# Optimization experiments

Measured on AMD Instinct MI355X. Metric: run time of the kernel, lower is better.

The kernel has to match this reference:

```python
import jax, jax.numpy as jnp
import numpy as np

B = 131072
D_IN = 385          # 384-d embedding + 1 correctness feature
D_H = 192           # both trunk layers resolve to max(.,192)=192 per source
Q = 1000            # number of questions
C = 16              # classes per head (uniform padding of per-question heads)


def setup_inputs() -> dict:
    key = jax.random.key(0)
    ks = jax.random.split(key, 9)
    x = jax.random.normal(ks[0], (B, D_IN), dtype=jnp.float32)
    question_ids = jax.random.randint(ks[1], (B,), 0, Q, dtype=jnp.int32)
    is_correct = jax.random.randint(ks[2], (B,), 0, 2, dtype=jnp.int32)
    W1 = jax.random.normal(ks[3], (D_IN, D_H), dtype=jnp.float32) * 0.05
    b1 = jnp.zeros((D_H,), dtype=jnp.float32)
    W2 = jax.random.normal(ks[4], (D_H, D_H), dtype=jnp.float32) * 0.05
    b2 = jnp.zeros((D_H,), dtype=jnp.float32)
    # Head bank: slots [0,Q) = false heads, [Q,2Q) = true heads.
    W_heads = jax.random.normal(ks[5], (2 * Q, C, D_H), dtype=jnp.float32) * 0.05
    b_heads = jax.random.normal(ks[6], (2 * Q, C), dtype=jnp.float32) * 0.05
    return {"x": x, "question_ids": question_ids, "is_correct": is_correct,
            "W1": W1, "b1": b1, "W2": W2, "b2": b2,
            "W_heads": W_heads, "b_heads": b_heads}


def reference(x, question_ids, is_correct, W1, b1, W2, b2, W_heads, b_heads):
    # Shared trunk (eval mode: dropout = identity)
    h = jax.nn.relu(x @ W1 + b1)            # [B, 192]
    feat = jax.nn.relu(h @ W2 + b2)         # [B, 192]
    # Hard routing: pick true or false head for this question.
    Qn = W_heads.shape[0] // 2
    idx = question_ids + is_correct * Qn    # [B]
    Wq = W_heads[idx]                       # [B, C, 192] gather (memory-bound)
    bq = b_heads[idx]                       # [B, C]
    logits = jnp.einsum('bcd,bd->bc', Wq, feat) + bq  # per-sample routed linear
    return logits
```

## Files before the change

### kernel.cpp

```cpp
#include <hip/hip_runtime.h>
#include <hip/hip_bf16.h>
#include <stdint.h>
#include <stddef.h>


typedef short s8v __attribute__((ext_vector_type(8)));
typedef float f4v __attribute__((ext_vector_type(4)));
typedef float f4a __attribute__((ext_vector_type(4), aligned(4)));

typedef const void __attribute__((address_space(1))) *gas1_t;
typedef void __attribute__((address_space(3))) *las3_t;

namespace {
constexpr int kDin = 385;
constexpr int kDh  = 192;
constexpr int kQ   = 1000;
constexpr int kC   = 16;
constexpr int BM   = 64;
constexpr int NT   = 256;
constexpr int NK1  = 13;
constexpr int NK2  = 6;
constexpr int CHUNK = 12 * 64 * 8;
constexpr int H2   = 200;

constexpr size_t WS_W1   = 0;
constexpr size_t WS_W2   = 163840;
constexpr size_t WS_HIST = 245760;
constexpr size_t WS_CUR  = 253952;
constexpr size_t WS_PERM = 262144;
}

__device__ __forceinline__ unsigned short f2bf(float f) {
  unsigned int u = __float_as_uint(f);
  u = u + 0x7fffu + ((u >> 16) & 1u);
  return (unsigned short)(u >> 16);
}

__device__ __forceinline__ unsigned int pk2(float lo, float hi) {
  union { __hip_bfloat162 h2; unsigned int u; } cv;
  cv.h2 = __float22bfloat162_rn(make_float2(lo, hi));
  return cv.u;
}

union s8u { s8v s; unsigned int u[4]; };

__device__ __forceinline__ void swz_one(const float* W, int K, int i,
                                        unsigned short* out) {
  int k = i / kDh;
  int c = i - k * kDh;
  float v = (k < K) ? W[(size_t)k * kDh + c] : 0.f;
  int oi = (k >> 5) * CHUNK + (((c >> 4) * 64 + ((k >> 3) & 3) * 16 + (c & 15)) << 3)
         + (k & 7);
  out[oi] = f2bf(v);
}

__global__ void combo_prep(const int* __restrict__ qid, const int* __restrict__ isc,
                           int B, int nbH,
                           const float* __restrict__ W1, const float* __restrict__ W2,
                           int* __restrict__ hist,
                           unsigned short* __restrict__ W1sw,
                           unsigned short* __restrict__ W2sw) {
  int bid = blockIdx.x;
  if (bid < nbH) {
    int i = bid * 256 + threadIdx.x;
    if (i < B) atomicAdd(&hist[qid[i] + isc[i] * kQ], 1);
  } else if (bid < nbH + 312) {
    swz_one(W1, kDin, (bid - nbH) * 256 + threadIdx.x, W1sw);
  } else {
    swz_one(W2, kDh, (bid - nbH - 312) * 256 + threadIdx.x, W2sw);
  }
}

__global__ __launch_bounds__(256)
void scatter2(const int* __restrict__ qid, const int* __restrict__ isc, int B,
              const int* __restrict__ hist, int* __restrict__ rank_ctr,
              int* __restrict__ perm) {
  __shared__ int sh[2048];
  __shared__ int ssum[256];
  int t = threadIdx.x;
  int4 a = ((const int4*)hist)[t * 2];
  int4 b = ((const int4*)hist)[t * 2 + 1];
  int s1 = a.x + a.y, s2 = s1 + a.z, s3 = s2 + a.w;
  int s4 = s3 + b.x, s5 = s4 + b.y, s6 = s5 + b.z, s7 = s6 + b.w;
  ssum[t] = s7;
  __syncthreads();
  #pragma unroll
  for (int d = 1; d < 256; d <<= 1) {
    int xv = (t >= d) ? ssum[t - d] : 0;
    __syncthreads();
    ssum[t] += xv;
    __syncthreads();
  }
  int base = ssum[t] - s7;
  sh[t * 8 + 0] = base;
  sh[t * 8 + 1] = base + a.x;
  sh[t * 8 + 2] = base + s1;
  sh[t * 8 + 3] = base + s2;
  sh[t * 8 + 4] = base + s3;
  sh[t * 8 + 5] = base + s4;
  sh[t * 8 + 6] = base + s5;
  sh[t * 8 + 7] = base + s6;
  __syncthreads();
  int i = blockIdx.x * 256 + t;
  if (i < B) {
    int h = qid[i] + isc[i] * kQ;
    int pos = sh[h] + atomicAdd(&rank_ctr[h], 1);
    perm[pos] = i;
  }
}

__device__ __forceinline__ void stage_chunk(const unsigned short* gsrc,
                                            unsigned short* lbase, int tid) {
  const char* g = (const char*)gsrc + (size_t)tid * 16;
  char* l = (char*)lbase + ((tid >> 6) << 10);
  __builtin_amdgcn_global_load_lds((gas1_t)g,          (las3_t)l,          16, 0, 0);
  __builtin_amdgcn_global_load_lds((gas1_t)(g + 4096), (las3_t)(l + 4096), 16, 0, 0);
  __builtin_amdgcn_global_load_lds((gas1_t)(g + 8192), (las3_t)(l + 8192), 16, 0, 0);
}

__global__ __launch_bounds__(NT, 3)
void fused_qmlp6(const float* __restrict__ x,
                 const int*   __restrict__ qid,
                 const int*   __restrict__ isc,
                 const float* __restrict__ b1,
                 const float* __restrict__ b2,
                 const float* __restrict__ Wh,
                 const float* __restrict__ bh,
                 const unsigned short* __restrict__ W1sw,
                 const unsigned short* __restrict__ W2sw,
                 const int*   __restrict__ perm,
                 float* __restrict__ out) {
  __shared__ __align__(16) unsigned short hS[BM * H2];
  __shared__ __align__(16) unsigned short bS[2 * CHUNK];
  __shared__ int permS[BM];
  __shared__ int idxS[BM];

  const int tid  = threadIdx.x;
  const int lane = tid & 63, wid = tid >> 6;
  const int m = lane & 15, quad = lane >> 4;
  const int rh = wid & 1, ch = wid >> 1;
  const int row0 = blockIdx.x * BM;

  if (tid < BM) {
    int p = perm[row0 + tid];
    permS[tid] = p;
    idxS[tid] = qid[p] + isc[p] * kQ;
  }
  stage_chunk(W1sw, bS, tid);
  __syncthreads();

  const float* px0 = x + (size_t)permS[rh * 32 + m] * kDin;
  const float* px1 = x + (size_t)permS[rh * 32 + m + 16] * kDin;

  f4v acc0[6], acc1[6];
  #pragma unroll
  for (int t = 0; t < 6; ++t) {
    acc0[t] = (f4v){0.f, 0.f, 0.f, 0.f};
    acc1[t] = (f4v){0.f, 0.f, 0.f, 0.f};
  }

  f4a c0, c1, c2, c3;
  {
    const float* q0 = px0 + quad * 8;
    const float* q1 = px1 + quad * 8;
    c0 = *(const f4a*)q0; c1 = *(const f4a*)(q0 + 4);
    c2 = *(const f4a*)q1; c3 = *(const f4a*)(q1 + 4);
  }
  float tl0 = 0.f, tl1 = 0.f;

  #pragma unroll
  for (int kk = 0; kk < NK1; ++kk) {
    const int nj = kk + 1;
    const unsigned short* np = (nj < NK1)
        ? W1sw + (size_t)nj * CHUNK
        : W2sw;
    stage_chunk(np, bS + (nj & 1) * CHUNK, tid);

    f4a n0, n1, n2, n3;
    if (kk < NK1 - 2) {
      const float* q0 = px0 + nj * 32 + quad * 8;
      const float* q1 = px1 + nj * 32 + quad * 8;
      n0 = *(const f4a*)q0; n1 = *(const f4a*)(q0 + 4);
      n2 = *(const f4a*)q1; n3 = *(const f4a*)(q1 + 4);
    } else if (kk == NK1 - 2) {
      tl0 = (quad == 0) ? px0[384] : 0.f;
      tl1 = (quad == 0) ? px1[384] : 0.f;
    }

    s8v a0, a1;
    if (kk < NK1 - 1) {
      s8u ua, ub;
      ua.u[0] = pk2(c0[0], c0[1]); ua.u[1] = pk2(c0[2], c0[3]);
      ua.u[2] = pk2(c1[0], c1[1]); ua.u[3] = pk2(c1[2], c1[3]);
      ub.u[0] = pk2(c2[0], c2[1]); ub.u[1] = pk2(c2[2], c2[3]);
      ub.u[2] = pk2(c3[0], c3[1]); ub.u[3] = pk2(c3[2], c3[3]);
      a0 = ua.s; a1 = ub.s;
    } else {
      a0 = (s8v){0,0,0,0,0,0,0,0};
      a1 = (s8v){0,0,0,0,0,0,0,0};
      a0[0] = (short)f2bf(tl0);
      a1[0] = (short)f2bf(tl1);
    }

    const unsigned short* bBuf = bS + (kk & 1) * CHUNK;
    #pragma unroll
    for (int t = 0; t < 6; ++t) {
      s8v b = *(const s8v*)&bBuf[((ch * 6 + t) * 64 + lane) * 8];
      acc0[t] = __builtin_amdgcn_mfma_f32_16x16x32_bf16(a0, b, acc0[t], 0, 0, 0);
      acc1[t] = __builtin_amdgcn_mfma_f32_16x16x32_bf16(a1, b, acc1[t], 0, 0, 0);
    }
    __syncthreads();
    if (kk < NK1 - 2) { c0 = n0; c1 = n1; c2 = n2; c3 = n3; }
  }

  #pragma unroll
  for (int t = 0; t < 6; ++t) {
    int c = ch * 96 + t * 16 + m;
    float bb = b1[c];
    #pragma unroll
    for (int r4 = 0; r4 < 4; ++r4) {
      int r = rh * 32 + quad * 4 + r4;
      float v0 = acc0[t][r4] + bb; v0 = v0 > 0.f ? v0 : 0.f;
      hS[r * H2 + c] = f2bf(v0);
      float v1 = acc1[t][r4] + bb; v1 = v1 > 0.f ? v1 : 0.f;
      hS[(r + 16) * H2 + c] = f2bf(v1);
      acc0[t][r4] = 0.f;
      acc1[t][r4] = 0.f;
    }
  }
  __syncthreads();

  const int ar0 = (rh * 32 + m) * H2;
  #pragma unroll
  for (int k2 = 0; k2 < NK2; ++k2) {
    if (k2 < NK2 - 1)
      stage_chunk(W2sw + (size_t)(k2 + 1) * CHUNK,
                  bS + ((14 + k2) & 1) * CHUNK, tid);

    s8v a0 = *(const s8v*)&hS[ar0 + k2 * 32 + quad * 8];
    s8v a1 = *(const s8v*)&hS[ar0 + 16 * H2 + k2 * 32 + quad * 8];
    const unsigned short* bBuf = bS + ((13 + k2) & 1) * CHUNK;
    #pragma unroll
    for (int t = 0; t < 6; ++t) {
      s8v b = *(const s8v*)&bBuf[((ch * 6 + t) * 64 + lane) * 8];
      acc0[t] = __builtin_amdgcn_mfma_f32_16x16x32_bf16(a0, b, acc0[t], 0, 0, 0);
      acc1[t] = __builtin_amdgcn_mfma_f32_16x16x32_bf16(a1, b, acc1[t], 0, 0, 0);
    }
    __syncthreads();
  }

  #pragma unroll
  for (int t = 0; t < 6; ++t) {
    int c = ch * 96 + t * 16 + m;
    float bb = b2[c];
    #pragma unroll
    for (int r4 = 0; r4 < 4; ++r4) {
      int r = rh * 32 + quad * 4 + r4;
      float v0 = acc0[t][r4] + bb;
      hS[r * H2 + c] = f2bf(v0 > 0.f ? v0 : 0.f);
      float v1 = acc1[t][r4] + bb;
      hS[(r + 16) * H2 + c] = f2bf(v1 > 0.f ? v1 : 0.f);
    }
  }
  __syncthreads();

  {
    const int w16 = wid * 16;
    const int hm = idxS[w16 + m];
    unsigned rem = 0xFFFFu;
    while (rem) {
      int r0 = (int)__builtin_ctz(rem);
      int h = idxS[w16 + r0];
      unsigned long long bal = __ballot(hm == h);
      unsigned mask16 = (unsigned)(bal & 0xFFFFu);
      rem &= ~mask16;
      bool valid = (hm == h);

      const float* wq = Wh + ((size_t)h * kC + m) * kDh + quad * 8;
      f4v acc = (f4v){0.f, 0.f, 0.f, 0.f};
      #pragma unroll
      for (int kk = 0; kk < 6; ++kk) {
        float4 wlo = *(const float4*)(wq + kk * 32);
        float4 whi = *(const float4*)(wq + kk * 32 + 4);
        s8u ub;
        ub.u[0] = pk2(wlo.x, wlo.y);
        ub.u[1] = pk2(wlo.z, wlo.w);
        ub.u[2] = pk2(whi.x, whi.y);
        ub.u[3] = pk2(whi.z, whi.w);
        s8v bfr = ub.s;
        s8v afr = *(const s8v*)&hS[(w16 + m) * H2 + kk * 32 + quad * 8];
        if (!valid) afr = (s8v){0,0,0,0,0,0,0,0};
        acc = __builtin_amdgcn_mfma_f32_16x16x32_bf16(afr, bfr, acc, 0, 0, 0);
      }
      float bhv = bh[(size_t)h * kC + m];
      #pragma unroll
      for (int reg = 0; reg < 4; ++reg) {
        int r = quad * 4 + reg;
        if ((mask16 >> r) & 1u)
          out[(size_t)permS[w16 + r] * kC + m] = acc[reg] + bhv;
      }
    }
  }
}

extern "C" void kernel_launch(void* const* d_in, const int* in_sizes, int n_in,
                              void* d_out, int out_size, void* d_ws, size_t ws_size,
                              hipStream_t stream) {
  const float* x  = (const float*)d_in[0];
  const int*   qd = (const int*)  d_in[1];
  const int*   ic = (const int*)  d_in[2];
  const float* W1 = (const float*)d_in[3];
  const float* b1 = (const float*)d_in[4];
  const float* W2 = (const float*)d_in[5];
  const float* b2 = (const float*)d_in[6];
  const float* Wh = (const float*)d_in[7];
  const float* bh = (const float*)d_in[8];
  float* out = (float*)d_out;

  char* ws = (char*)d_ws;
  unsigned short* W1sw = (unsigned short*)(ws + WS_W1);
  unsigned short* W2sw = (unsigned short*)(ws + WS_W2);
  int* hist = (int*)(ws + WS_HIST);
  int* rank = (int*)(ws + WS_CUR);
  int* perm = (int*)(ws + WS_PERM);

  int B = in_sizes[1];
  int nbH = (B + 255) / 256;

  hipMemsetAsync(hist, 0, 4096 * sizeof(int), stream);
  combo_prep<<<nbH + 312 + 144, 256, 0, stream>>>(qd, ic, B, nbH, W1, W2,
                                                  hist, W1sw, W2sw);
  scatter2<<<(B + 255) / 256, 256, 0, stream>>>(qd, ic, B, hist, rank, perm);

  fused_qmlp6<<<B / BM, NT, 0, stream>>>(x, qd, ic, b1, b2, Wh, bh,
                                         W1sw, W2sw, perm, out);
}
```

Before: 413.1 us.

## Use 8 waves per block with single-buffered weight staging and split head work

Doubles threads per block to 512, so each wave computes 16 rows instead of 32 and holds half as many accumulators. Weight chunks are now single-buffered in LDS, with the next chunk staged after a barrier, to cut LDS use and allow more resident blocks (launch bounds raised to 8). In the routed-head phase, runs of same-head rows are alternated between the two column-half waves. The trade-off is that weight loads no longer overlap with MFMA work, and each k-step needs two barriers, which adds sync overhead.

```diff
diff --git a/kernel.cpp b/kernel.cpp
--- a/kernel.cpp
+++ b/kernel.cpp
@@ -17,7 +17,7 @@
 constexpr int kQ   = 1000;
 constexpr int kC   = 16;
 constexpr int BM   = 64;
-constexpr int NT   = 256;
+constexpr int NT   = 512;
 constexpr int NK1  = 13;
 constexpr int NK2  = 6;
 constexpr int CHUNK = 12 * 64 * 8;
@@ -109,17 +109,8 @@
   }
 }
 
-__device__ __forceinline__ void stage_chunk(const unsigned short* gsrc,
-                                            unsigned short* lbase, int tid) {
-  const char* g = (const char*)gsrc + (size_t)tid * 16;
-  char* l = (char*)lbase + ((tid >> 6) << 10);
-  __builtin_amdgcn_global_load_lds((gas1_t)g,          (las3_t)l,          16, 0, 0);
-  __builtin_amdgcn_global_load_lds((gas1_t)(g + 4096), (las3_t)(l + 4096), 16, 0, 0);
-  __builtin_amdgcn_global_load_lds((gas1_t)(g + 8192), (las3_t)(l + 8192), 16, 0, 0);
-}
-
-__global__ __launch_bounds__(NT, 3)
-void fused_qmlp6(const float* __restrict__ x,
+__global__ __launch_bounds__(NT, 8)
+void fused_qmlp8(const float* __restrict__ x,
                  const int*   __restrict__ qid,
                  const int*   __restrict__ isc,
                  const float* __restrict__ b1,
@@ -131,174 +122,165 @@
                  const int*   __restrict__ perm,
                  float* __restrict__ out) {
   __shared__ __align__(16) unsigned short hS[BM * H2];
-  __shared__ __align__(16) unsigned short bS[2 * CHUNK];
+  __shared__ __align__(16) unsigned short bS[CHUNK];
   __shared__ int permS[BM];
   __shared__ int idxS[BM];
 
   const int tid  = threadIdx.x;
   const int lane = tid & 63, wid = tid >> 6;
   const int m = lane & 15, quad = lane >> 4;
-  const int rh = wid & 1, ch = wid >> 1;
+  const int rh = wid >> 1, ch = wid & 1;
   const int row0 = blockIdx.x * BM;
 
+  {
+    const char* g = (const char*)W1sw + (size_t)tid * 16;
+    char* l = (char*)bS + ((tid >> 6) << 10);
+    __builtin_amdgcn_global_load_lds((gas1_t)g, (las3_t)l, 16, 0, 0);
+    if (tid < 256)
+      __builtin_amdgcn_global_load_lds((gas1_t)(g + 8192), (las3_t)(l + 8192),
+                                       16, 0, 0);
+  }
   if (tid < BM) {
     int p = perm[row0 + tid];
     permS[tid] = p;
     idxS[tid] = qid[p] + isc[p] * kQ;
   }
-  stage_chunk(W1sw, bS, tid);
   __syncthreads();
 
-  const float* px0 = x + (size_t)permS[rh * 32 + m] * kDin;
-  const float* px1 = x + (size_t)permS[rh * 32 + m + 16] * kDin;
-
-  f4v acc0[6], acc1[6];
+  const float* px = x + (size_t)permS[rh * 16 + m] * kDin;
+
+  f4v acc[6];
   #pragma unroll
-  for (int t = 0; t < 6; ++t) {
-    acc0[t] = (f4v){0.f, 0.f, 0.f, 0.f};
-    acc1[t] = (f4v){0.f, 0.f, 0.f, 0.f};
-  }
-
-  f4a c0, c1, c2, c3;
-  {
-    const float* q0 = px0 + quad * 8;
-    const float* q1 = px1 + quad * 8;
-    c0 = *(const f4a*)q0; c1 = *(const f4a*)(q0 + 4);
-    c2 = *(const f4a*)q1; c3 = *(const f4a*)(q1 + 4);
-  }
-  float tl0 = 0.f, tl1 = 0.f;
+  for (int t = 0; t < 6; ++t) acc[t] = (f4v){0.f, 0.f, 0.f, 0.f};
+
+  f4a c0 = *(const f4a*)(px + quad * 8);
+  f4a c1 = *(const f4a*)(px + quad * 8 + 4);
+  float tl = 0.f;
 
   #pragma unroll
   for (int kk = 0; kk < NK1; ++kk) {
-    const int nj = kk + 1;
-    const unsigned short* np = (nj < NK1)
-        ? W1sw + (size_t)nj * CHUNK
-        : W2sw;
-    stage_chunk(np, bS + (nj & 1) * CHUNK, tid);
-
-    f4a n0, n1, n2, n3;
-    if (kk < NK1 - 2) {
-      const float* q0 = px0 + nj * 32 + quad * 8;
-      const float* q1 = px1 + nj * 32 + quad * 8;
-      n0 = *(const f4a*)q0; n1 = *(const f4a*)(q0 + 4);
-      n2 = *(const f4a*)q1; n3 = *(const f4a*)(q1 + 4);
-    } else if (kk == NK1 - 2) {
-      tl0 = (quad == 0) ? px0[384] : 0.f;
-      tl1 = (quad == 0) ? px1[384] : 0.f;
-    }
-
-    s8v a0, a1;
+    s8v a;
     if (kk < NK1 - 1) {
-      s8u ua, ub;
+      s8u ua;
       ua.u[0] = pk2(c0[0], c0[1]); ua.u[1] = pk2(c0[2], c0[3]);
       ua.u[2] = pk2(c1[0], c1[1]); ua.u[3] = pk2(c1[2], c1[3]);
-      ub.u[0] = pk2(c2[0], c2[1]); ub.u[1] = pk2(c2[2], c2[3]);
-      ub.u[2] = pk2(c3[0], c3[1]); ub.u[3] = pk2(c3[2], c3[3]);
-      a0 = ua.s; a1 = ub.s;
+      a = ua.s;
     } else {
-      a0 = (s8v){0,0,0,0,0,0,0,0};
-      a1 = (s8v){0,0,0,0,0,0,0,0};
-      a0[0] = (short)f2bf(tl0);
-      a1[0] = (short)f2bf(tl1);
-    }
-
-    const unsigned short* bBuf = bS + (kk & 1) * CHUNK;
+      a = (s8v){0,0,0,0,0,0,0,0};
+      a[0] = (short)f2bf(tl);
+    }
+
     #pragma unroll
     for (int t = 0; t < 6; ++t) {
-      s8v b = *(const s8v*)&bBuf[((ch * 6 + t) * 64 + lane) * 8];
-      acc0[t] = __builtin_amdgcn_mfma_f32_16x16x32_bf16(a0, b, acc0[t], 0, 0, 0);
-      acc1[t] = __builtin_amdgcn_mfma_f32_16x16x32_bf16(a1, b, acc1[t], 0, 0, 0);
-    }
-    __syncthreads();
-    if (kk < NK1 - 2) { c0 = n0; c1 = n1; c2 = n2; c3 = n3; }
-  }
-
-  #pragma unroll
-  for (int t = 0; t < 6; ++t) {
-    int c = ch * 96 + t * 16 + m;
-    float bb = b1[c];
-    #pragma unroll
-    for (int r4 = 0; r4 < 4; ++r4) {
-      int r = rh * 32 + quad * 4 + r4;
-      float v0 = acc0[t][r4] + bb; v0 = v0 > 0.f ? v0 : 0.f;
-      hS[r * H2 + c] = f2bf(v0);
-      float v1 = acc1[t][r4] + bb; v1 = v1 > 0.f ? v1 : 0.f;
-      hS[(r + 16) * H2 + c] = f2bf(v1);
-      acc0[t][r4] = 0.f;
-      acc1[t][r4] = 0.f;
-    }
-  }
-  __syncthreads();
-
-  const int ar0 = (rh * 32 + m) * H2;
+      s8v b = *(const s8v*)&bS[((ch * 6 + t) * 64 + lane) * 8];
+      acc[t] = __builtin_amdgcn_mfma_f32_16x16x32_bf16(a, b, acc[t], 0, 0, 0);
+    }
+    __syncthreads();
+
+    {
+      const unsigned short* np = (kk < NK1 - 1)
+          ? W1sw + (size_t)(kk + 1) * CHUNK : W2sw;
+      const char* g = (const char*)np + (size_t)tid * 16;
+      char* l = (char*)bS + ((tid >> 6) << 10);
+      __builtin_amdgcn_global_load_lds((gas1_t)g, (las3_t)l, 16, 0, 0);
+      if (tid < 256)
+        __builtin_amdgcn_global_load_lds((gas1_t)(g + 8192), (las3_t)(l + 8192),
+                                         16, 0, 0);
+    }
+    if (kk < NK1 - 2) {
+      c0 = *(const f4a*)(px + (kk + 1) * 32 + quad * 8);
+      c1 = *(const f4a*)(px + (kk + 1) * 32 + quad * 8 + 4);
+    } else if (kk == NK1 - 2) {
+      tl = (quad == 0) ? px[384] : 0.f;
+    }
+    if (kk == NK1 - 1) {
+      #pragma unroll
+      for (int t = 0; t < 6; ++t) {
+        int c = ch * 96 + t * 16 + m;
+        float bb = b1[c];
+        #pragma unroll
+        for (int r4 = 0; r4 < 4; ++r4) {
+          int r = rh * 16 + quad * 4 + r4;
+          float v0 = acc[t][r4] + bb;
+          hS[r * H2 + c] = f2bf(v0 > 0.f ? v0 : 0.f);
+          acc[t][r4] = 0.f;
+        }
+      }
+    }
+    __syncthreads();
+  }
+
+  const int ar0 = (rh * 16 + m) * H2;
   #pragma unroll
   for (int k2 = 0; k2 < NK2; ++k2) {
-    if (k2 < NK2 - 1)
-      stage_chunk(W2sw + (size_t)(k2 + 1) * CHUNK,
-                  bS + ((14 + k2) & 1) * CHUNK, tid);
-
-    s8v a0 = *(const s8v*)&hS[ar0 + k2 * 32 + quad * 8];
-    s8v a1 = *(const s8v*)&hS[ar0 + 16 * H2 + k2 * 32 + quad * 8];
-    const unsigned short* bBuf = bS + ((13 + k2) & 1) * CHUNK;
+    s8v a = *(const s8v*)&hS[ar0 + k2 * 32 + quad * 8];
     #pragma unroll
     for (int t = 0; t < 6; ++t) {
-      s8v b = *(const s8v*)&bBuf[((ch * 6 + t) * 64 + lane) * 8];
-      acc0[t] = __builtin_amdgcn_mfma_f32_16x16x32_bf16(a0, b, acc0[t], 0, 0, 0);
-      acc1[t] = __builtin_amdgcn_mfma_f32_16x16x32_bf16(a1, b, acc1[t], 0, 0, 0);
-    }
-    __syncthreads();
-  }
-
-  #pragma unroll
-  for (int t = 0; t < 6; ++t) {
-    int c = ch * 96 + t * 16 + m;
-    float bb = b2[c];
-    #pragma unroll
-    for (int r4 = 0; r4 < 4; ++r4) {
-      int r = rh * 32 + quad * 4 + r4;
-      float v0 = acc0[t][r4] + bb;
-      hS[r * H2 + c] = f2bf(v0 > 0.f ? v0 : 0.f);
-      float v1 = acc1[t][r4] + bb;
-      hS[(r + 16) * H2 + c] = f2bf(v1 > 0.f ? v1 : 0.f);
-    }
-  }
-  __syncthreads();
+      s8v b = *(const s8v*)&bS[((ch * 6 + t) * 64 + lane) * 8];
+      acc[t] = __builtin_amdgcn_mfma_f32_16x16x32_bf16(a, b, acc[t], 0, 0, 0);
+    }
+    __syncthreads();
+    if (k2 < NK2 - 1) {
+      const char* g = (const char*)(W2sw + (size_t)(k2 + 1) * CHUNK)
+                    + (size_t)tid * 16;
+      char* l = (char*)bS + ((tid >> 6) << 10);
+      __builtin_amdgcn_global_load_lds((gas1_t)g, (las3_t)l, 16, 0, 0);
+      if (tid < 256)
+        __builtin_amdgcn_global_load_lds((gas1_t)(g + 8192), (las3_t)(l + 8192),
+                                         16, 0, 0);
+    } else {
+      #pragma unroll
+      for (int t = 0; t < 6; ++t) {
+        int c = ch * 96 + t * 16 + m;
+        float bb = b2[c];
+        #pragma unroll
+        for (int r4 = 0; r4 < 4; ++r4) {
+          int r = rh * 16 + quad * 4 + r4;
+          float v0 = acc[t][r4] + bb;
+          hS[r * H2 + c] = f2bf(v0 > 0.f ? v0 : 0.f);
+        }
+      }
+    }
+    __syncthreads();
+  }
 
   {
-    const int w16 = wid * 16;
+    const int w16 = rh * 16;
     const int hm = idxS[w16 + m];
     unsigned rem = 0xFFFFu;
+    int runIdx = 0;
     while (rem) {
       int r0 = (int)__builtin_ctz(rem);
       int h = idxS[w16 + r0];
       unsigned long long bal = __ballot(hm == h);
       unsigned mask16 = (unsigned)(bal & 0xFFFFu);
       rem &= ~mask16;
-      bool valid = (hm == h);
-
-      const float* wq = Wh + ((size_t)h * kC + m) * kDh + quad * 8;
-      f4v acc = (f4v){0.f, 0.f, 0.f, 0.f};
-      #pragma unroll
-      for (int kk = 0; kk < 6; ++kk) {
-        float4 wlo = *(const float4*)(wq + kk * 32);
-        float4 whi = *(const float4*)(wq + kk * 32 + 4);
-        s8u ub;
-        ub.u[0] = pk2(wlo.x, wlo.y);
-        ub.u[1] = pk2(wlo.z, wlo.w);
-        ub.u[2] = pk2(whi.x, whi.y);
-        ub.u[3] = pk2(whi.z, whi.w);
-        s8v bfr = ub.s;
-        s8v afr = *(const s8v*)&hS[(w16 + m) * H2 + kk * 32 + quad * 8];
-        if (!valid) afr = (s8v){0,0,0,0,0,0,0,0};
-        acc = __builtin_amdgcn_mfma_f32_16x16x32_bf16(afr, bfr, acc, 0, 0, 0);
+      if ((runIdx & 1) == ch) {
+        const float* wq = Wh + ((size_t)h * kC + m) * kDh + quad * 8;
+        f4v acch = (f4v){0.f, 0.f, 0.f, 0.f};
+        #pragma unroll
+        for (int kk = 0; kk < 6; ++kk) {
+          float4 wlo = *(const float4*)(wq + kk * 32);
+          float4 whi = *(const float4*)(wq + kk * 32 + 4);
+          s8u ub;
+          ub.u[0] = pk2(wlo.x, wlo.y);
+          ub.u[1] = pk2(wlo.z, wlo.w);
+          ub.u[2] = pk2(whi.x, whi.y);
+          ub.u[3] = pk2(whi.z, whi.w);
+          s8v bfr = ub.s;
+          s8v afr = *(const s8v*)&hS[(w16 + m) * H2 + kk * 32 + quad * 8];
+          if (hm != h) afr = (s8v){0,0,0,0,0,0,0,0};
+          acch = __builtin_amdgcn_mfma_f32_16x16x32_bf16(afr, bfr, acch, 0, 0, 0);
+        }
+        float bhv = bh[(size_t)h * kC + m];
+        #pragma unroll
+        for (int reg = 0; reg < 4; ++reg) {
+          int r = quad * 4 + reg;
+          if ((mask16 >> r) & 1u)
+            out[(size_t)permS[w16 + r] * kC + m] = acch[reg] + bhv;
+        }
       }
-      float bhv = bh[(size_t)h * kC + m];
-      #pragma unroll
-      for (int reg = 0; reg < 4; ++reg) {
-        int r = quad * 4 + reg;
-        if ((mask16 >> r) & 1u)
-          out[(size_t)permS[w16 + r] * kC + m] = acc[reg] + bhv;
-      }
+      runIdx++;
     }
   }
 }
@@ -332,6 +314,6 @@
                                                   hist, W1sw, W2sw);
   scatter2<<<(B + 255) / 256, 256, 0, stream>>>(qd, ic, B, hist, rank, perm);
 
-  fused_qmlp6<<<B / BM, NT, 0, stream>>>(x, qd, ic, b1, b2, Wh, bh,
+  fused_qmlp8<<<B / BM, NT, 0, stream>>>(x, qd, ic, b1, b2, Wh, bh,
                                          W1sw, W2sw, perm, out);
 }
```

Result: faster. 392.0 us (-5.1%).
